# Optimization experiments

Hardware: AMD Instinct MI355X
Metric: run time of the kernel (lower is better)

The kernel has to match this reference:

```python
import jax, jax.numpy as jnp
import numpy as np

B, N, DIM = 2, 4096, 1024
HEADS, DH, W = 16, 64, 512
INNER = int(DIM * 2 * 4 / 3)  # 2730 (GEGLU FeedForward, mult=4)


def setup_inputs() -> dict:
    key = jax.random.key(0)
    ks = jax.random.split(key, 6)
    rn = lambda k, shape, sc: jax.random.normal(k, shape, jnp.float32) * sc
    return {
        "x": rn(ks[0], (B, N, DIM), 1.0),
        "ln1_w": jnp.ones((DIM,), jnp.float32),
        "ln1_b": jnp.zeros((DIM,), jnp.float32),
        "w_qkv": rn(ks[1], (DIM, 3 * HEADS * DH), 0.02),
        "w_out": rn(ks[2], (HEADS * DH, DIM), 0.02),
        "ln2_w": jnp.ones((DIM,), jnp.float32),
        "w_ff1": rn(ks[3], (DIM, 2 * INNER), 0.02),
        "w_ff2": rn(ks[4], (INNER, DIM), 0.02),
    }


def _layernorm(x, w, b=None, eps=1e-5):
    m = x.mean(-1, keepdims=True)
    v = x.var(-1, keepdims=True)
    y = (x - m) * jax.lax.rsqrt(v + eps) * w
    return y + b if b is not None else y


def _rotary_freqs(n, d):
    inv = 1.0 / (10000.0 ** (jnp.arange(0, d, 2, dtype=jnp.float32) / d))
    f = jnp.arange(n, dtype=jnp.float32)[:, None] * inv[None, :]  # [n, d/2]
    return jnp.concatenate([f, f], axis=-1)  # [n, d]


def _rotate_half(x):
    x1, x2 = jnp.split(x, 2, axis=-1)
    return jnp.concatenate([-x2, x1], axis=-1)


def _apply_rotary(x, freqs):
    return x * jnp.cos(freqs) + _rotate_half(x) * jnp.sin(freqs)


def reference(x, ln1_w, ln1_b, w_qkv, w_out, ln2_w, w_ff1, w_ff2):
    # ---- LocalMHA (prenorm, causal windowed attention, look_backward=1) ----
    h = _layernorm(x, ln1_w, ln1_b)
    qkv = h @ w_qkv  # [b, n, 3*h*d]
    q, k, v = jnp.split(qkv, 3, axis=-1)
    to_heads = lambda t: t.reshape(B, N, HEADS, DH).transpose(0, 2, 1, 3)  # [b,h,n,d]
    q, k, v = map(to_heads, (q, k, v))

    freqs = _rotary_freqs(N, DH)  # [n, d]
    q = _apply_rotary(q, freqs)
    k = _apply_rotary(k, freqs)
    q = q * (DH ** -0.5)

    nw = N // W
    bq = q.reshape(B, HEADS, nw, W, DH)
    bk = k.reshape(B, HEADS, nw, W, DH)
    bv = v.reshape(B, HEADS, nw, W, DH)

    def look_back(t):  # prepend previous window (zeros for first window)
        prev = jnp.concatenate([jnp.zeros_like(t[:, :, :1]), t[:, :, :-1]], axis=2)
        return jnp.concatenate([prev, t], axis=3)  # [b,h,nw,2w,d]

    kk, vv = look_back(bk), look_back(bv)

    tq = jnp.arange(N).reshape(nw, W)
    tprev = jnp.concatenate([jnp.full((1, W), -1, tq.dtype), tq[:-1]], axis=0)
    tk = jnp.concatenate([tprev, tq], axis=1)  # [nw, 2w]
    mask = (tq[:, :, None] >= tk[:, None, :]) & (tk[:, None, :] >= 0)  # causal + pad

    sim = jnp.einsum('bhnqd,bhnkd->bhnqk', bq, kk)
    sim = jnp.where(mask, sim, jnp.finfo(sim.dtype).min / 2)
    attn = jax.nn.softmax(sim, axis=-1)
    o = jnp.einsum('bhnqk,bhnkd->bhnqd', attn, vv)
    o = o.reshape(B, HEADS, N, DH).transpose(0, 2, 1, 3).reshape(B, N, HEADS * DH)
    x = o @ w_out + x  # residual

    # ---- FeedForward: LN(gamma only) -> GEGLU -> Linear, residual ----
    h = _layernorm(x, ln2_w)
    u = h @ w_ff1
    a, g = jnp.split(u, 2, axis=-1)
    x = (a * jax.nn.gelu(g, approximate=False)) @ w_ff2 + x
    return x
```

## Files before the change

### kernel.cpp

```cpp
#include <hip/hip_runtime.h>
#include <stdint.h>

typedef unsigned short u16;
typedef unsigned int u32;

#define BATCH 2
#define NSEQ  4096
#define DIM   1024
#define HEADS 16
#define DH    64
#define WIN   512
#define INNER 2730
#define ROWS  8192
#define QKV_N 3072
#define FF1_N 5460
#define FF1_NP 5632
#define INNER_P 2816
#define KROT 0.28782313663f

typedef __attribute__((ext_vector_type(8))) short short8;
typedef __attribute__((ext_vector_type(4))) float float4v;

__device__ __forceinline__ float bf2f(u16 u){ union{u32 i;float f;}c; c.i=((u32)u)<<16; return c.f; }
__device__ __forceinline__ u16 f2bf(float f){ union{float f;u32 i;}c; c.f=f; u32 i=c.i;
    return (u16)((i + 0x7FFFu + ((i>>16)&1u))>>16); }

__device__ __forceinline__ float gelu_fast(float g) {
    float t = 0.7978845608f * (g + 0.044715f * g * g * g);
    float th = 1.f - 2.f / (1.f + __expf(2.f * t));
    return 0.5f * g * (1.f + th);
}

__device__ __forceinline__ void gl_lds16(const u16* g, const u16* ldsbase) {
    __builtin_amdgcn_global_load_lds(
        (const __attribute__((address_space(1))) u32*)(uintptr_t)g,
        (__attribute__((address_space(3))) u32*)(uintptr_t)ldsbase,
        16, 0, 0);
}

__device__ __forceinline__ int ff1_src(int n, bool& ok) {
    int t = n >> 7, m = n & 127, j = m >> 4, l = m & 15;
    int p = t * 64 + ((j >> 1) << 4) + l;
    ok = (p < INNER);
    return (j & 1) ? (INNER + p) : p;
}

template <bool REMAP>
__global__ __launch_bounds__(256) void wtrans_kernel(const float* __restrict__ w, u16* __restrict__ wt,
                                                     int K0, int N0, int K1, int N1) {
    __shared__ float tile[32][33];
    int kt = blockIdx.x, nt = blockIdx.y;
    int tx = threadIdx.x & 31, ty = threadIdx.x >> 5;
    int nl = nt * 32 + tx;
    bool ok = (nl < N1);
    int sc = nl;
    if (REMAP) { bool v; sc = ff1_src(nl < N1 ? nl : 0, v); ok = ok && v; }
    else ok = ok && (nl < N0);
#pragma unroll
    for (int yy = 0; yy < 4; yy++) {
        int k = kt*32 + ty + yy*8;
        tile[ty+yy*8][tx] = (k < K0 && ok) ? w[(size_t)k*N0 + sc] : 0.f;
    }
    __syncthreads();
#pragma unroll
    for (int yy = 0; yy < 4; yy++) {
        int n = nt*32 + ty + yy*8, k = kt*32 + tx;
        if (n < N1 && k < K1) wt[(size_t)n*K1 + k] = f2bf(tile[tx][ty+yy*8]);
    }
}

__global__ __launch_bounds__(256) void ln_kernel(const float* __restrict__ x,
                                                 const float* __restrict__ w,
                                                 const float* __restrict__ b,
                                                 u16* __restrict__ out) {
    int row = blockIdx.x;
    const float* xr = x + (size_t)row * DIM;
    int t = threadIdx.x;
    float v[4];
    float s = 0.f, s2 = 0.f;
#pragma unroll
    for (int i = 0; i < 4; i++) {
        float f = xr[t + 256 * i];
        v[i] = f; s += f; s2 += f * f;
    }
#pragma unroll
    for (int off = 32; off; off >>= 1) { s += __shfl_xor(s, off); s2 += __shfl_xor(s2, off); }
    __shared__ float ls[10];
    int wave = t >> 6, lane = t & 63;
    if (lane == 0) { ls[wave] = s; ls[4 + wave] = s2; }
    __syncthreads();
    if (t == 0) {
        float ts  = ls[0] + ls[1] + ls[2] + ls[3];
        float ts2 = ls[4] + ls[5] + ls[6] + ls[7];
        float mean = ts * (1.f / DIM);
        float var  = ts2 * (1.f / DIM) - mean * mean;
        ls[8] = mean; ls[9] = 1.f / sqrtf(var + 1e-5f);
    }
    __syncthreads();
    float mean = ls[8], inv = ls[9];
    u16* orow = out + (size_t)row * DIM;
#pragma unroll
    for (int i = 0; i < 4; i++) {
        int c = t + 256 * i;
        float y = (v[i] - mean) * inv * w[c];
        if (b) y += b[c];
        orow[c] = f2bf(y);
    }
}

template <int MODE>
__global__ __launch_bounds__(512, 2) void gemm256(const u16* __restrict__ A,
                                                  const u16* __restrict__ Bt,
                                                  void* __restrict__ Cv,
                                                  int N, int K) {
    extern __shared__ u16 lds[];
    u16* Asm = lds;
    u16* Bsm = lds + 4 * 8192;
    int tiles_n = N >> 8;
    int gs  = tiles_n << 3;
    int gid = blockIdx.x / gs;
    int loc = blockIdx.x % gs;
    int tm = gid * 8 + (loc & 7);
    int tn = loc >> 3;
    int tid = threadIdx.x, wave = tid >> 6, lane = tid & 63;
    int quad = lane >> 4, l15 = lane & 15;
    int wm = wave >> 2, wn = wave & 3;
    int srow = wave * 16 + (lane >> 2);
    int sgrp = (lane & 3) ^ ((srow >> 1) & 3);
    const u16* Ag = A  + (size_t)(tm * 256 + srow) * K + sgrp * 8;
    const u16* Bg = Bt + (size_t)(tn * 256 + srow) * K + sgrp * 8;
    u16* Asw = Asm + wave * 512;
    u16* Bsw = Bsm + wave * 512;
    int rg = (l15 >> 1) & 3;
    int nk = K >> 5;

    float4v acc[8][4];
#pragma unroll
    for (int i = 0; i < 8; i++)
#pragma unroll
        for (int j = 0; j < 4; j++) acc[i][j] = (float4v){0.f, 0.f, 0.f, 0.f};

    auto stage = [&](int t) {
        int b = t & 3;
        int k0 = t << 5;
        gl_lds16(Ag + k0,                   Asw + b * 8192);
        gl_lds16(Ag + (size_t)128 * K + k0, Asw + b * 8192 + 4096);
        gl_lds16(Bg + k0,                   Bsw + b * 8192);
        gl_lds16(Bg + (size_t)128 * K + k0, Bsw + b * 8192 + 4096);
    };
    auto compute = [&](int t) {
        const u16* Ab = Asm + (t & 3) * 8192;
        const u16* Bb = Bsm + (t & 3) * 8192;
        short8 af[8], bfr[4];
#pragma unroll
        for (int i = 0; i < 8; i++)
            af[i] = *(const short8*)&Ab[(wm*128 + i*16 + l15) * 32 + ((quad ^ rg) * 8)];
#pragma unroll
        for (int j = 0; j < 4; j++)
            bfr[j] = *(const short8*)&Bb[(wn*64 + j*16 + l15) * 32 + ((quad ^ rg) * 8)];
        __builtin_amdgcn_s_setprio(1);
#pragma unroll
        for (int i = 0; i < 8; i++)
#pragma unroll
            for (int j = 0; j < 4; j++)
                acc[i][j] = __builtin_amdgcn_mfma_f32_16x16x32_bf16(af[i], bfr[j], acc[i][j], 0, 0, 0);
        __builtin_amdgcn_s_setprio(0);
    };

    stage(0); stage(1); stage(2);

#define KSTEP(T, VM) \
    asm volatile("s_waitcnt vmcnt(" #VM ")" ::: "memory"); \
    __builtin_amdgcn_s_barrier(); \
    __builtin_amdgcn_sched_barrier(0); \
    compute(T); \
    if ((T) + 3 < nk) stage((T) + 3);

    for (int t = 0; t < nk - 2; ++t) { KSTEP(t, 8); }
    { KSTEP(nk - 2, 4); }
    { KSTEP(nk - 1, 0); }
#undef KSTEP

    if (MODE == 2) {
        u16* C = (u16*)Cv;
        int sector = tn >> 2;
        if (sector < 2) {
            float inv0 = __expf(-(float)l15 * KROT);
            float inv1 = __expf(-(float)(l15 + 16) * KROT);
            float sc = (sector == 0) ? 0.125f : 1.0f;
#pragma unroll
            for (int i = 0; i < 8; i++) {
#pragma unroll
                for (int r = 0; r < 4; r++) {
                    int row = tm*256 + wm*128 + i*16 + quad*4 + r;
                    float fn = (float)(row & (NSEQ - 1));
                    float s0, c0, s1, c1;
                    __sincosf(fn * inv0, &s0, &c0);
                    __sincosf(fn * inv1, &s1, &c1);
                    float a0 = acc[i][0][r], a1 = acc[i][1][r];
                    float a2 = acc[i][2][r], a3 = acc[i][3][r];
                    size_t base = (size_t)row * N + tn*256 + wn*64 + l15;
                    C[base]      = f2bf((a0*c0 - a2*s0) * sc);
                    C[base + 16] = f2bf((a1*c1 - a3*s1) * sc);
                    C[base + 32] = f2bf((a2*c0 + a0*s0) * sc);
                    C[base + 48] = f2bf((a3*c1 + a1*s1) * sc);
                }
            }
        } else {
#pragma unroll
            for (int i = 0; i < 8; i++)
#pragma unroll
                for (int r = 0; r < 4; r++) {
                    size_t base = (size_t)(tm*256 + wm*128 + i*16 + quad*4 + r) * N + tn*256 + wn*64 + l15;
#pragma unroll
                    for (int j = 0; j < 4; j++) C[base + j*16] = f2bf(acc[i][j][r]);
                }
        }
        return;
    }
    if (MODE == 3) {
        u16* ag = (u16*)Cv;
        int t128 = tn * 2 + (wn >> 1);
        int cb = t128 * 64 + (wn & 1) * 32;
#pragma unroll
        for (int i = 0; i < 8; i++) {
#pragma unroll
            for (int r = 0; r < 4; r++) {
                size_t row = (size_t)(tm*256 + wm*128 + i*16 + quad*4 + r);
#pragma unroll
                for (int jp = 0; jp < 2; jp++) {
                    float a = acc[i][2*jp][r];
                    float g = acc[i][2*jp+1][r];
                    int col = cb + jp*16 + l15;
                    ag[row * INNER_P + col] = f2bf(a * gelu_fast(g));
                }
            }
        }
        return;
    }
}

template <int MODE>
__global__ __launch_bounds__(256) void gemm_tile(const u16* __restrict__ A,
                                                 const u16* __restrict__ Bt,
                                                 const float* __restrict__ resid,
                                                 void* __restrict__ Cv,
                                                 int M, int N, int K) {
    __shared__ u16 As[2][128 * 32];
    __shared__ u16 Bs[2][128 * 32];
    int tiles_n = N >> 7;
    int gs  = tiles_n << 3;
    int gid = blockIdx.x / gs;
    int loc = blockIdx.x % gs;
    int tm = gid * 8 + (loc & 7);
    int tn = loc >> 3;
    int tid = threadIdx.x, wave = tid >> 6, lane = tid & 63;
    int quad = lane >> 4, l15 = lane & 15;
    int wm = wave >> 1, wn = wave & 1;
    int srow = wave * 32 + (lane >> 2);
    int sgrp = (lane & 3) ^ ((srow >> 1) & 3);
    const u16* Ag = A  + (size_t)(tm * 128 + srow) * K + sgrp * 8;
    const u16* Bg = Bt + (size_t)(tn * 128 + srow) * K + sgrp * 8;
    const u16* Alb0 = &As[0][wave * 1024];
    const u16* Blb0 = &Bs[0][wave * 1024];
    const u16* Alb1 = &As[1][wave * 1024];
    const u16* Blb1 = &Bs[1][wave * 1024];
    int rg = (l15 >> 1) & 3;
    float4v acc[4][4];
#pragma unroll
    for (int i = 0; i < 4; i++)
#pragma unroll
        for (int j = 0; j < 4; j++) acc[i][j] = (float4v){0.f, 0.f, 0.f, 0.f};

    gl_lds16(Ag,                Alb0);
    gl_lds16(Ag + (size_t)16*K, Alb0 + 512);
    gl_lds16(Bg,                Blb0);
    gl_lds16(Bg + (size_t)16*K, Blb0 + 512);
    __syncthreads();

    int nk = K >> 5;
    for (int t = 0; t < nk; ++t) {
        int buf = t & 1;
        if (t + 1 < nk) {
            int k0 = (t + 1) << 5;
            const u16* Al = buf ? Alb0 : Alb1;
            const u16* Bl = buf ? Blb0 : Blb1;
            gl_lds16(Ag + k0,                Al);
            gl_lds16(Ag + (size_t)16*K + k0, Al + 512);
            gl_lds16(Bg + k0,                Bl);
            gl_lds16(Bg + (size_t)16*K + k0, Bl + 512);
        }
        const u16* Asb = &As[buf][0];
        const u16* Bsb = &Bs[buf][0];
        short8 af[4], bf[4];
#pragma unroll
        for (int i = 0; i < 4; i++)
            af[i] = *(const short8*)&Asb[(wm*64 + i*16 + l15)*32 + ((quad ^ rg) * 8)];
#pragma unroll
        for (int j = 0; j < 4; j++)
            bf[j] = *(const short8*)&Bsb[(wn*64 + j*16 + l15)*32 + ((quad ^ rg) * 8)];
#pragma unroll
        for (int i = 0; i < 4; i++)
#pragma unroll
            for (int j = 0; j < 4; j++)
                acc[i][j] = __builtin_amdgcn_mfma_f32_16x16x32_bf16(af[i], bf[j], acc[i][j], 0, 0, 0);
        __syncthreads();
    }
#pragma unroll
    for (int i = 0; i < 4; i++) {
#pragma unroll
        for (int r = 0; r < 4; r++) {
            size_t row = (size_t)(tm*128 + wm*64 + i*16 + quad*4 + r);
#pragma unroll
            for (int j = 0; j < 4; j++) {
                int col = tn*128 + wn*64 + j*16 + l15;
                size_t idx = row * N + col;
                float v = acc[i][j][r];
                if (MODE == 1) { if (resid) v += resid[idx]; ((float*)Cv)[idx] = v; }
                else ((u16*)Cv)[idx] = f2bf(v);
            }
        }
    }
}

__global__ __launch_bounds__(256) void vtrans_kernel(const u16* __restrict__ qkv, u16* __restrict__ vt) {
    __shared__ u16 tile[64][72];
    int t = threadIdx.x;
    int n0 = (blockIdx.x & 63) * 64;
    int hh = (blockIdx.x >> 6) & 15;
    int b  = blockIdx.x >> 10;
    int r = t >> 2, cb = (t & 3) * 16;
    const u16* src = qkv + (size_t)(b * NSEQ + n0 + r) * QKV_N + 2 * DIM + hh * 64 + cb;
    uint4 v0 = *(const uint4*)(src);
    uint4 v1 = *(const uint4*)(src + 8);
    *(uint4*)&tile[r][cb]     = v0;
    *(uint4*)&tile[r][cb + 8] = v1;
    __syncthreads();
    int d = t >> 2, nb = (t & 3) * 16;
    __align__(16) u16 vals[16];
#pragma unroll
    for (int e = 0; e < 16; e++) vals[e] = tile[nb + e][d];
    u16* dst = vt + ((size_t)(b * HEADS + hh) * DH + d) * NSEQ + n0 + nb;
    *(uint4*)(dst)     = *(uint4*)&vals[0];
    *(uint4*)(dst + 8) = *(uint4*)&vals[8];
}

__global__ __launch_bounds__(256) void attn_kernel(const u16* __restrict__ qkv,
                                                   const u16* __restrict__ vt,
                                                   u16* __restrict__ o) {
    __shared__ u16 Ks[128 * 64];
    __shared__ u16 Vs[64 * 128];
    __shared__ u16 p_lds[4][16][136];
    int tid = threadIdx.x, wave = tid >> 6, lane = tid & 63;
    int quad = lane >> 4, l15 = lane & 15;
    int bi = blockIdx.x;
    int qb = bi & 7, w0 = (bi >> 3) & 7, hh = (bi >> 6) & 15, b = bi >> 10;
    int qt = qb * 4 + wave;
    int qlocal = qt * 16 + l15;
    const u16* qp = qkv + (size_t)(b*NSEQ + w0*WIN + qt*16 + l15) * QKV_N + hh*64 + quad*8;
    short8 bq0 = *(const short8*)(qp);
    short8 bq1 = *(const short8*)(qp + 32);
    int krow0 = b * NSEQ + (w0 - 1) * WIN;
    const u16* vbase = vt + (size_t)(b * HEADS + hh) * DH * NSEQ + (w0 - 1) * WIN;
    int ks_row = lane >> 3;
    int ks_g   = (lane & 7) ^ ks_row;
    int vs_row = lane >> 4;
    int vs_j0  = lane & 15;
    int swz = l15 & 7;
    float m_ = -1e30f, l_ = 0.f;
    float4v O[4] = {{0,0,0,0},{0,0,0,0},{0,0,0,0},{0,0,0,0}};
    int cstart = (w0 == 0) ? 4 : 0;
    int clast  = (512 + qb * 64 + 63) >> 7;
    u16 (*pt)[136] = p_lds[wave];
    for (int c = cstart; c <= clast; c++) {
        int kb = c * 128;
        __syncthreads();
#pragma unroll
        for (int i = 0; i < 4; i++) {
            int kloc = wave * 32 + i * 8 + ks_row;
            gl_lds16(qkv + (size_t)(krow0 + kb + kloc) * QKV_N + DIM + hh*64 + ks_g*8,
                     &Ks[(wave*32 + i*8) * 64]);
        }
#pragma unroll
        for (int i = 0; i < 4; i++) {
            int dloc = wave * 16 + i * 4 + vs_row;
            int jsrc = vs_j0 ^ (dloc & 7);
            gl_lds16(vbase + (size_t)dloc * NSEQ + kb + jsrc * 8,
                     &Vs[(wave*16 + i*4) * 128]);
        }
        __syncthreads();
        float4v s[8];
#pragma unroll
        for (int t = 0; t < 8; t++) {
            int krow = (t*16 + l15) * 64;
            short8 ka0 = *(const short8*)&Ks[krow + ((quad    ) ^ swz) * 8];
            short8 ka1 = *(const short8*)&Ks[krow + ((quad + 4) ^ swz) * 8];
            float4v st = {0.f, 0.f, 0.f, 0.f};
            st = __builtin_amdgcn_mfma_f32_16x16x32_bf16(ka0, bq0, st, 0, 0, 0);
            st = __builtin_amdgcn_mfma_f32_16x16x32_bf16(ka1, bq1, st, 0, 0, 0);
            int ck = kb + t*16 + quad*4;
#pragma unroll
            for (int r = 0; r < 4; r++)
                if (ck + r >= 512 && ck + r - 512 > qlocal) st[r] = -1e30f;
            s[t] = st;
        }
        float mc = -1e30f;
#pragma unroll
        for (int t = 0; t < 8; t++)
#pragma unroll
            for (int r = 0; r < 4; r++) mc = fmaxf(mc, s[t][r]);
        mc = fmaxf(mc, __shfl_xor(mc, 16));
        mc = fmaxf(mc, __shfl_xor(mc, 32));
        float mn = fmaxf(m_, mc);
        float alpha = __expf(m_ - mn);
        m_ = mn;
        float su = 0.f;
#pragma unroll
        for (int t = 0; t < 8; t++) {
            union { u16 h[4]; uint2 v; } pk;
#pragma unroll
            for (int r = 0; r < 4; r++) {
                float p = __expf(s[t][r] - mn);
                su += p;
                pk.h[r] = f2bf(p);
            }
            *(uint2*)&pt[l15][t*16 + quad*4] = pk.v;
        }
        su += __shfl_xor(su, 16);
        su += __shfl_xor(su, 32);
        l_ = l_ * alpha + su;
#pragma unroll
        for (int t = 0; t < 4; t++)
#pragma unroll
            for (int r = 0; r < 4; r++) O[t][r] *= alpha;
#pragma unroll
        for (int g = 0; g < 4; g++) {
            short8 pf = *(const short8*)&pt[l15][g*32 + quad*8];
#pragma unroll
            for (int t = 0; t < 4; t++) {
                short8 vf = *(const short8*)&Vs[(t*16 + l15) * 128 + ((g*4 + quad) ^ swz) * 8];
                O[t] = __builtin_amdgcn_mfma_f32_16x16x32_bf16(vf, pf, O[t], 0, 0, 0);
            }
        }
    }
    float inv = 1.f / l_;
    u16* op = o + (size_t)(b*NSEQ + w0*WIN + qt*16 + l15) * DIM + hh*64;
#pragma unroll
    for (int t = 0; t < 4; t++) {
        union { u16 h[4]; uint2 v; } pk;
#pragma unroll
        for (int r = 0; r < 4; r++) pk.h[r] = f2bf(O[t][r] * inv);
        *(uint2*)(op + t*16 + quad*4) = pk.v;
    }
}

extern "C" void kernel_launch(void* const* d_in, const int* in_sizes, int n_in,
                              void* d_out, int out_size, void* d_ws, size_t ws_size,
                              hipStream_t stream) {
    const float* x      = (const float*)d_in[0];
    const float* ln1_w  = (const float*)d_in[1];
    const float* ln1_b  = (const float*)d_in[2];
    const float* w_qkv  = (const float*)d_in[3];
    const float* w_out  = (const float*)d_in[4];
    const float* ln2_w  = (const float*)d_in[5];
    const float* w_ff1  = (const float*)d_in[6];
    const float* w_ff2  = (const float*)d_in[7];
    float* out = (float*)d_out;

    static bool cfg = false;
    if (!cfg) {
        hipFuncSetAttribute((const void*)gemm256<2>, hipFuncAttributeMaxDynamicSharedMemorySize, 131072);
        hipFuncSetAttribute((const void*)gemm256<3>, hipFuncAttributeMaxDynamicSharedMemorySize, 131072);
        cfg = true;
    }

    char* ws = (char*)d_ws;
    size_t off = 0;
    auto alloc = [&](size_t bytes) { size_t o = off; off += (bytes + 255) & ~(size_t)255; return o; };
    size_t off_wqt  = alloc((size_t)QKV_N  * DIM * 2);
    size_t off_wot  = alloc((size_t)DIM    * DIM * 2);
    size_t off_wf1t = alloc((size_t)FF1_NP * DIM * 2);
    size_t off_wf2t = alloc((size_t)DIM    * INNER_P * 2);
    size_t off_h    = alloc((size_t)ROWS * DIM * 2);
    size_t sz_qkv = (size_t)ROWS * QKV_N * 2;
    size_t sz_vt  = (size_t)BATCH * HEADS * DH * NSEQ * 2;
    size_t off_qkv  = alloc(sz_qkv);
    size_t off_vt   = alloc(sz_vt);
    size_t off_o    = alloc((size_t)ROWS * DIM * 2);
    size_t off_x1   = alloc((size_t)ROWS * DIM * 4);
    size_t off_ag   = alloc((size_t)ROWS * INNER_P * 2);

    u16* wqt  = (u16*)(ws + off_wqt);
    u16* wot  = (u16*)(ws + off_wot);
    u16* wf1t = (u16*)(ws + off_wf1t);
    u16* wf2t = (u16*)(ws + off_wf2t);
    u16* h    = (u16*)(ws + off_h);
    u16* qkv  = (u16*)(ws + off_qkv);
    u16* vt   = (u16*)(ws + off_vt);
    u16* o    = (u16*)(ws + off_o);
    float* x1 = (float*)(ws + off_x1);
    u16* ag   = (u16*)(ws + off_ag);

    wtrans_kernel<false><<<dim3(32, 96),  256, 0, stream>>>(w_qkv, wqt,  DIM,   QKV_N, DIM,     QKV_N);
    wtrans_kernel<false><<<dim3(32, 32),  256, 0, stream>>>(w_out, wot,  DIM,   DIM,   DIM,     DIM);
    wtrans_kernel<true ><<<dim3(32, 176), 256, 0, stream>>>(w_ff1, wf1t, DIM,   FF1_N, DIM,     FF1_NP);
    wtrans_kernel<false><<<dim3(88, 32),  256, 0, stream>>>(w_ff2, wf2t, INNER, DIM,   INNER_P, DIM);

    ln_kernel<<<ROWS, 256, 0, stream>>>(x, ln1_w, ln1_b, h);
    gemm256<2><<<(ROWS/256) * (QKV_N/256), 512, 131072, stream>>>(h, wqt, qkv, QKV_N, DIM);
    vtrans_kernel<<<BATCH * HEADS * (NSEQ / 64), 256, 0, stream>>>(qkv, vt);
    attn_kernel<<<BATCH * HEADS * 8 * 8, 256, 0, stream>>>(qkv, vt, o);
    gemm_tile<1><<<(ROWS/128) * (DIM/128), 256, 0, stream>>>(o, wot, x, x1, ROWS, DIM, DIM);
    ln_kernel<<<ROWS, 256, 0, stream>>>(x1, ln2_w, nullptr, h);
    gemm256<3><<<(ROWS/256) * (FF1_NP/256), 512, 131072, stream>>>(h, wf1t, ag, FF1_NP, DIM);
    gemm_tile<1><<<(ROWS/128) * (DIM/128), 256, 0, stream>>>(ag, wf2t, x1, out, ROWS, DIM, INNER_P);

    (void)in_sizes; (void)n_in; (void)out_size; (void)ws_size;
}
```

Before: 537.7 us.

## Split GEMM k-step into two half-phases interleaving LDS loads, prefetch, and MFMA

Restructures the bf16 GEMM main loop so each k-step runs in two halves. Each half reads part of the A fragments from LDS, issues half of the next global-to-LDS prefetch (A in the first half, B in the second), then runs half of the MFMAs. The aim is to overlap LDS reads and global prefetch issue with matrix-core work instead of loading everything up front. In exchange it adds extra workgroup barriers and lgkmcnt waits per k-step, which could cost more than the overlap gains.

```diff
diff --git a/kernel.cpp b/kernel.cpp
--- a/kernel.cpp
+++ b/kernel.cpp
@@ -140,46 +140,70 @@
 #pragma unroll
         for (int j = 0; j < 4; j++) acc[i][j] = (float4v){0.f, 0.f, 0.f, 0.f};
 
-    auto stage = [&](int t) {
+    auto stage2 = [&](int t, int h) {
         int b = t & 3;
         int k0 = t << 5;
-        gl_lds16(Ag + k0,                   Asw + b * 8192);
-        gl_lds16(Ag + (size_t)128 * K + k0, Asw + b * 8192 + 4096);
-        gl_lds16(Bg + k0,                   Bsw + b * 8192);
-        gl_lds16(Bg + (size_t)128 * K + k0, Bsw + b * 8192 + 4096);
+        if (h == 0) {
+            gl_lds16(Ag + k0,                   Asw + b * 8192);
+            gl_lds16(Ag + (size_t)128 * K + k0, Asw + b * 8192 + 4096);
+        } else {
+            gl_lds16(Bg + k0,                   Bsw + b * 8192);
+            gl_lds16(Bg + (size_t)128 * K + k0, Bsw + b * 8192 + 4096);
+        }
     };
-    auto compute = [&](int t) {
+    auto ldsA = [&](int t, int i) -> short8 {
         const u16* Ab = Asm + (t & 3) * 8192;
+        return *(const short8*)&Ab[(wm*128 + i*16 + l15) * 32 + ((quad ^ rg) * 8)];
+    };
+    auto ldsB = [&](int t, int j) -> short8 {
         const u16* Bb = Bsm + (t & 3) * 8192;
+        return *(const short8*)&Bb[(wn*64 + j*16 + l15) * 32 + ((quad ^ rg) * 8)];
+    };
+
+    stage2(0, 0); stage2(0, 1);
+    stage2(1, 0); stage2(1, 1);
+    stage2(2, 0); stage2(2, 1);
+    asm volatile("s_waitcnt vmcnt(8)" ::: "memory");
+    __builtin_amdgcn_s_barrier();
+
+    for (int t = 0; t < nk; ++t) {
         short8 af[8], bfr[4];
 #pragma unroll
-        for (int i = 0; i < 8; i++)
-            af[i] = *(const short8*)&Ab[(wm*128 + i*16 + l15) * 32 + ((quad ^ rg) * 8)];
-#pragma unroll
-        for (int j = 0; j < 4; j++)
-            bfr[j] = *(const short8*)&Bb[(wn*64 + j*16 + l15) * 32 + ((quad ^ rg) * 8)];
+        for (int i = 0; i < 4; i++) af[i] = ldsA(t, i);
+#pragma unroll
+        for (int j = 0; j < 4; j++) bfr[j] = ldsB(t, j);
+        if (t + 3 < nk) stage2(t + 3, 0);
+        __builtin_amdgcn_s_barrier();
+        asm volatile("s_waitcnt lgkmcnt(0)" ::: "memory");
+        __builtin_amdgcn_sched_barrier(0);
         __builtin_amdgcn_s_setprio(1);
 #pragma unroll
-        for (int i = 0; i < 8; i++)
+        for (int i = 0; i < 4; i++)
 #pragma unroll
             for (int j = 0; j < 4; j++)
                 acc[i][j] = __builtin_amdgcn_mfma_f32_16x16x32_bf16(af[i], bfr[j], acc[i][j], 0, 0, 0);
         __builtin_amdgcn_s_setprio(0);
-    };
-
-    stage(0); stage(1); stage(2);
-
-#define KSTEP(T, VM) \
-    asm volatile("s_waitcnt vmcnt(" #VM ")" ::: "memory"); \
-    __builtin_amdgcn_s_barrier(); \
-    __builtin_amdgcn_sched_barrier(0); \
-    compute(T); \
-    if ((T) + 3 < nk) stage((T) + 3);
-
-    for (int t = 0; t < nk - 2; ++t) { KSTEP(t, 8); }
-    { KSTEP(nk - 2, 4); }
-    { KSTEP(nk - 1, 0); }
-#undef KSTEP
+        __builtin_amdgcn_s_barrier();
+#pragma unroll
+        for (int i = 4; i < 8; i++) af[i] = ldsA(t, i);
+        if (t + 3 < nk) stage2(t + 3, 1);
+        __builtin_amdgcn_s_barrier();
+        asm volatile("s_waitcnt lgkmcnt(0)" ::: "memory");
+        __builtin_amdgcn_sched_barrier(0);
+        __builtin_amdgcn_s_setprio(1);
+#pragma unroll
+        for (int i = 4; i < 8; i++)
+#pragma unroll
+            for (int j = 0; j < 4; j++)
+                acc[i][j] = __builtin_amdgcn_mfma_f32_16x16x32_bf16(af[i], bfr[j], acc[i][j], 0, 0, 0);
+        __builtin_amdgcn_s_setprio(0);
+        if (t < nk - 1) {
+            if (t < nk - 3)       asm volatile("s_waitcnt vmcnt(8)" ::: "memory");
+            else if (t == nk - 3) asm volatile("s_waitcnt vmcnt(4)" ::: "memory");
+            else                  asm volatile("s_waitcnt vmcnt(0)" ::: "memory");
+            __builtin_amdgcn_s_barrier();
+        }
+    }
 
     if (MODE == 2) {
         u16* C = (u16*)Cv;
```

After: 544.0 us. About the same (+1.2%).
